# Optimization experiments

Hardware: AMD Instinct MI355X
Metric: run time of the kernel (lower is better)

The kernel has to match this reference:

```python
import jax, jax.numpy as jnp
import numpy as np

N = 1_000_000
IN_DIM = 256
HIDDEN = 32
NUM_SEG = 100_000


def setup_inputs() -> dict:
    key = jax.random.key(0)
    ks = jax.random.split(key, 6)
    review_x = jax.random.normal(ks[0], (N, IN_DIM), dtype=jnp.float32)
    Wq = jax.random.normal(ks[1], (IN_DIM, HIDDEN), dtype=jnp.float32) * (1.0 / np.sqrt(IN_DIM))
    bq = jax.random.normal(ks[2], (HIDDEN,), dtype=jnp.float32) * 0.01
    Wk = jax.random.normal(ks[3], (IN_DIM, HIDDEN), dtype=jnp.float32) * (1.0 / np.sqrt(IN_DIM))
    bk = jax.random.normal(ks[4], (HIDDEN,), dtype=jnp.float32) * 0.01
    review_to_rest_idx = jax.random.randint(ks[5], (N,), 0, NUM_SEG, dtype=jnp.int64 if jax.config.jax_enable_x64 else jnp.int32)
    return {
        "review_x": review_x,
        "Wq": Wq,
        "bq": bq,
        "Wk": Wk,
        "bk": bk,
        "review_to_rest_idx": review_to_rest_idx,
        "num_segments": NUM_SEG,
    }


def reference(review_x, Wq, bq, Wk, bk, review_to_rest_idx, num_segments):
    # q/k projections: [N, hidden]
    qv = review_x @ Wq + bq
    kv = review_x @ Wk + bk
    # attention logits per review: [N]
    att = jnp.sum(qv * kv, axis=-1)
    idx = review_to_rest_idx
    # segment softmax (numerically stable): max, exp, sum per restaurant group
    seg_max = jax.ops.segment_max(att, idx, num_segments=num_segments)
    # empty segments yield -inf max; never gathered, but keep finite for safety
    seg_max = jnp.where(jnp.isfinite(seg_max), seg_max, 0.0)
    e = jnp.exp(att - seg_max[idx])
    seg_sum = jax.ops.segment_sum(e, idx, num_segments=num_segments)
    weights = e / seg_sum[idx]
    return weights
```

## Files before the change

### kernel.cpp

```cpp
#include <hip/hip_runtime.h>
#include <hip/hip_fp16.h>
#include <math.h>

#define IN_DIM 256
#define HID 32
#define NSEG 100000
#define ROWB 1024
#define WBUF 16384

typedef _Float16 half8 __attribute__((ext_vector_type(8)));
typedef __fp16  fp16x2 __attribute__((ext_vector_type(2)));
typedef float floatx4 __attribute__((ext_vector_type(4)));

__device__ __forceinline__ void gload_lds16(const float* g, char* l) {
    __builtin_amdgcn_global_load_lds(
        (const __attribute__((address_space(1))) void*)g,
        (__attribute__((address_space(3))) void*)l,
        16, 0, 0);
}

__global__ __launch_bounds__(256, 2) void att_kernel(
    const float* __restrict__ x,
    const float* __restrict__ Wq, const float* __restrict__ bq,
    const float* __restrict__ Wk, const float* __restrict__ bk,
    const int* __restrict__ idx,
    float* __restrict__ e_out, float* __restrict__ segsum,
    int n, int nsub)
{
    extern __shared__ char smem[];

    const int tid = threadIdx.x;
    const int w  = tid >> 6, l = tid & 63;
    const int lr = l & 15,  lg = l >> 4;

    {
        _Float16* BF = (_Float16*)smem;
        const int ks = tid >> 5, lg2 = (tid >> 3) & 3, j = tid & 7;
        const float4* wqr = (const float4*)(Wq + (size_t)tid * HID);
        const float4* wkr = (const float4*)(Wk + (size_t)tid * HID);
#pragma unroll
        for (int i = 0; i < 8; ++i) {
            float4 vq = wqr[i];
            float4 vk = wkr[i];
            float fq[4] = { vq.x, vq.y, vq.z, vq.w };
            float fk[4] = { vk.x, vk.y, vk.z, vk.w };
#pragma unroll
            for (int u2 = 0; u2 < 4; ++u2) {
                int c = i * 4 + u2, cg = c >> 4, cr = c & 15;
                BF[(((cg    ) * 8 + ks) * 64 + lg2 * 16 + cr) * 8 + j] = (_Float16)fq[u2];
                BF[(((cg + 2) * 8 + ks) * 64 + lg2 * 16 + cr) * 8 + j] = (_Float16)fk[u2];
            }
        }
    }
    __syncthreads();
    half8 b[4][8];
    {
        const _Float16* bfl = (const _Float16*)smem + (size_t)l * 8;
#pragma unroll
        for (int cg = 0; cg < 4; ++cg)
#pragma unroll
            for (int ks = 0; ks < 8; ++ks)
                b[cg][ks] = *(const half8*)(bfl + (cg * 8 + ks) * 512);
    }
    __syncthreads();

    const float bq0 = bq[lr], bq1 = bq[lr + 16];
    const float bk0 = bk[lr], bk1 = bk[lr + 16];

    char* const Xw = smem + w * WBUF;
    const char* const Xr = Xw + lr * ROWB;
    const int sw = lr & 7;

    auto stage = [&](int s) {
#pragma unroll
        for (int r = 0; r < 16; ++r) {
            int grow = s * 16 + r;
            if (grow >= n) grow = n - 1;
            const float* src = x + (size_t)grow * IN_DIM + ((l ^ (r & 7)) << 2);
            gload_lds16(src, Xw + r * ROWB);
        }
    };

    const int gw      = blockIdx.x * 4 + w;
    const int gstride = gridDim.x * 4;

    int s = gw;
    if (s >= nsub) return;

    stage(s);

    while (true) {
        asm volatile("s_waitcnt vmcnt(0)" ::: "memory");
        __builtin_amdgcn_sched_barrier(0);

        floatx4 acc0 = {0.f,0.f,0.f,0.f}, acc1 = {0.f,0.f,0.f,0.f};
        floatx4 acc2 = {0.f,0.f,0.f,0.f}, acc3 = {0.f,0.f,0.f,0.f};
#pragma unroll
        for (int ks = 0; ks < 8; ++ks) {
            float4 v0 = *(const float4*)(Xr + ks * 128 + (((lg * 2 + 0) ^ sw) << 4));
            float4 v1 = *(const float4*)(Xr + ks * 128 + (((lg * 2 + 1) ^ sw) << 4));
            union { half8 h8; fp16x2 h2[4]; } u;
            u.h2[0] = __builtin_amdgcn_cvt_pkrtz(v0.x, v0.y);
            u.h2[1] = __builtin_amdgcn_cvt_pkrtz(v0.z, v0.w);
            u.h2[2] = __builtin_amdgcn_cvt_pkrtz(v1.x, v1.y);
            u.h2[3] = __builtin_amdgcn_cvt_pkrtz(v1.z, v1.w);
            acc0 = __builtin_amdgcn_mfma_f32_16x16x32_f16(u.h8, b[0][ks], acc0, 0, 0, 0);
            acc1 = __builtin_amdgcn_mfma_f32_16x16x32_f16(u.h8, b[1][ks], acc1, 0, 0, 0);
            acc2 = __builtin_amdgcn_mfma_f32_16x16x32_f16(u.h8, b[2][ks], acc2, 0, 0, 0);
            acc3 = __builtin_amdgcn_mfma_f32_16x16x32_f16(u.h8, b[3][ks], acc3, 0, 0, 0);
        }

        float p[4];
#pragma unroll
        for (int i2 = 0; i2 < 4; ++i2) {
            p[i2] = (acc0[i2] + bq0) * (acc2[i2] + bk0)
                  + (acc1[i2] + bq1) * (acc3[i2] + bk1);
            p[i2] += __shfl_xor(p[i2], 1);
            p[i2] += __shfl_xor(p[i2], 2);
            p[i2] += __shfl_xor(p[i2], 4);
            p[i2] += __shfl_xor(p[i2], 8);
        }

        const int snext = s + gstride;

        asm volatile("s_waitcnt lgkmcnt(0)" ::: "memory");
        __builtin_amdgcn_sched_barrier(0);

        if (snext < nsub) stage(snext);

        if (lr < 4) {
            float pv = (lr & 1) ? ((lr & 2) ? p[3] : p[1])
                                : ((lr & 2) ? p[2] : p[0]);
            int r = s * 16 + lg * 4 + lr;
            if (r < n) {
                float e = __expf(pv);
                e_out[r] = e;
                atomicAdd(&segsum[idx[r]], e);
            }
        }

        if (snext >= nsub) break;
        s = snext;
    }
}

__global__ __launch_bounds__(256) void norm_kernel(
    const int* __restrict__ idx, const float* __restrict__ segsum,
    float* __restrict__ out, int n)
{
    int i = blockIdx.x * blockDim.x + threadIdx.x;
    int stride = gridDim.x * blockDim.x;
    int n4 = n >> 2;
    for (; i < n4; i += stride) {
        float4 e = ((const float4*)out)[i];
        int4  s4 = ((const int4*)idx)[i];
        float4 r;
        r.x = e.x / segsum[s4.x];
        r.y = e.y / segsum[s4.y];
        r.z = e.z / segsum[s4.z];
        r.w = e.w / segsum[s4.w];
        ((float4*)out)[i] = r;
    }
    if (blockIdx.x == 0 && threadIdx.x < (n & 3)) {
        int j = (n & ~3) + threadIdx.x;
        out[j] = out[j] / segsum[idx[j]];
    }
}

extern "C" void kernel_launch(void* const* d_in, const int* in_sizes, int n_in,
                              void* d_out, int out_size, void* d_ws, size_t ws_size,
                              hipStream_t stream)
{
    const float* x   = (const float*)d_in[0];
    const float* Wq  = (const float*)d_in[1];
    const float* bq  = (const float*)d_in[2];
    const float* Wk  = (const float*)d_in[3];
    const float* bk  = (const float*)d_in[4];
    const int*   idx = (const int*)d_in[5];
    const int n = in_sizes[5];

    float* segsum = (float*)d_ws;

    (void)hipMemsetAsync(segsum, 0, (size_t)NSEG * 4, stream);

    const int nsub = (n + 15) >> 4;
    int grid1 = 512;
    if (grid1 * 4 > nsub) grid1 = (nsub + 3) / 4;
    att_kernel<<<grid1, 256, 65536, stream>>>(x, Wq, bq, Wk, bk, idx,
                                              (float*)d_out, segsum, n, nsub);

    int n4 = n >> 2;
    int grid2 = (n4 + 255) / 256;
    if (grid2 > 1024) grid2 = 1024;
    if (grid2 < 1) grid2 = 1;
    norm_kernel<<<grid2, 256, 0, stream>>>(idx, segsum, (float*)d_out, n);
}
```

Before: 222.6 us.

## Load activations directly into registers with a software prefetch instead of LDS staging

Replaces the global-to-LDS async staging of x rows with direct global loads into a 16-entry float4 register buffer. The next subtile is prefetched into registers after the current one is converted to fp16. This drops 64KB of dynamic shared memory and the LDS read/wait round trip. In exchange it raises register pressure, and each lane now reads two strided 32-byte chunks per row, which may lower coalescing efficiency.

```diff
diff --git a/kernel.cpp b/kernel.cpp
--- a/kernel.cpp
+++ b/kernel.cpp
@@ -5,19 +5,10 @@
 #define IN_DIM 256
 #define HID 32
 #define NSEG 100000
-#define ROWB 1024
-#define WBUF 16384
 
 typedef _Float16 half8 __attribute__((ext_vector_type(8)));
 typedef __fp16  fp16x2 __attribute__((ext_vector_type(2)));
 typedef float floatx4 __attribute__((ext_vector_type(4)));
-
-__device__ __forceinline__ void gload_lds16(const float* g, char* l) {
-    __builtin_amdgcn_global_load_lds(
-        (const __attribute__((address_space(1))) void*)g,
-        (__attribute__((address_space(3))) void*)l,
-        16, 0, 0);
-}
 
 __global__ __launch_bounds__(256, 2) void att_kernel(
     const float* __restrict__ x,
@@ -27,14 +18,13 @@
     float* __restrict__ e_out, float* __restrict__ segsum,
     int n, int nsub)
 {
-    extern __shared__ char smem[];
+    __shared__ _Float16 BF[4 * 8 * 64 * 8];
 
     const int tid = threadIdx.x;
     const int w  = tid >> 6, l = tid & 63;
     const int lr = l & 15,  lg = l >> 4;
 
     {
-        _Float16* BF = (_Float16*)smem;
         const int ks = tid >> 5, lg2 = (tid >> 3) & 3, j = tid & 7;
         const float4* wqr = (const float4*)(Wq + (size_t)tid * HID);
         const float4* wkr = (const float4*)(Wk + (size_t)tid * HID);
@@ -55,31 +45,16 @@
     __syncthreads();
     half8 b[4][8];
     {
-        const _Float16* bfl = (const _Float16*)smem + (size_t)l * 8;
+        const _Float16* bfl = BF + (size_t)l * 8;
 #pragma unroll
         for (int cg = 0; cg < 4; ++cg)
 #pragma unroll
             for (int ks = 0; ks < 8; ++ks)
                 b[cg][ks] = *(const half8*)(bfl + (cg * 8 + ks) * 512);
     }
-    __syncthreads();
 
     const float bq0 = bq[lr], bq1 = bq[lr + 16];
     const float bk0 = bk[lr], bk1 = bk[lr + 16];
-
-    char* const Xw = smem + w * WBUF;
-    const char* const Xr = Xw + lr * ROWB;
-    const int sw = lr & 7;
-
-    auto stage = [&](int s) {
-#pragma unroll
-        for (int r = 0; r < 16; ++r) {
-            int grow = s * 16 + r;
-            if (grow >= n) grow = n - 1;
-            const float* src = x + (size_t)grow * IN_DIM + ((l ^ (r & 7)) << 2);
-            gload_lds16(src, Xw + r * ROWB);
-        }
-    };
 
     const int gw      = blockIdx.x * 4 + w;
     const int gstride = gridDim.x * 4;
@@ -87,27 +62,51 @@
     int s = gw;
     if (s >= nsub) return;
 
-    stage(s);
+    float4 raw[16];
+    {
+        int row = s * 16 + lr; if (row >= n) row = n - 1;
+        const float* xp = x + (size_t)row * IN_DIM + lg * 8;
+#pragma unroll
+        for (int ks = 0; ks < 8; ++ks) {
+            raw[2 * ks]     = *(const float4*)(xp + ks * 32);
+            raw[2 * ks + 1] = *(const float4*)(xp + ks * 32 + 4);
+        }
+    }
 
     while (true) {
-        asm volatile("s_waitcnt vmcnt(0)" ::: "memory");
+        const int snext = s + gstride;
+
+        half8 a[8];
+#pragma unroll
+        for (int ks = 0; ks < 8; ++ks) {
+            float4 v0 = raw[2 * ks], v1 = raw[2 * ks + 1];
+            union { half8 h8; fp16x2 h2[4]; } u;
+            u.h2[0] = __builtin_amdgcn_cvt_pkrtz(v0.x, v0.y);
+            u.h2[1] = __builtin_amdgcn_cvt_pkrtz(v0.z, v0.w);
+            u.h2[2] = __builtin_amdgcn_cvt_pkrtz(v1.x, v1.y);
+            u.h2[3] = __builtin_amdgcn_cvt_pkrtz(v1.z, v1.w);
+            a[ks] = u.h8;
+        }
+
+        if (snext < nsub) {
+            int row = snext * 16 + lr; if (row >= n) row = n - 1;
+            const float* xp = x + (size_t)row * IN_DIM + lg * 8;
+#pragma unroll
+            for (int ks = 0; ks < 8; ++ks) {
+                raw[2 * ks]     = *(const float4*)(xp + ks * 32);
+                raw[2 * ks + 1] = *(const float4*)(xp + ks * 32 + 4);
+            }
+        }
         __builtin_amdgcn_sched_barrier(0);
 
         floatx4 acc0 = {0.f,0.f,0.f,0.f}, acc1 = {0.f,0.f,0.f,0.f};
         floatx4 acc2 = {0.f,0.f,0.f,0.f}, acc3 = {0.f,0.f,0.f,0.f};
 #pragma unroll
         for (int ks = 0; ks < 8; ++ks) {
-            float4 v0 = *(const float4*)(Xr + ks * 128 + (((lg * 2 + 0) ^ sw) << 4));
-            float4 v1 = *(const float4*)(Xr + ks * 128 + (((lg * 2 + 1) ^ sw) << 4));
-            union { half8 h8; fp16x2 h2[4]; } u;
-            u.h2[0] = __builtin_amdgcn_cvt_pkrtz(v0.x, v0.y);
-            u.h2[1] = __builtin_amdgcn_cvt_pkrtz(v0.z, v0.w);
-            u.h2[2] = __builtin_amdgcn_cvt_pkrtz(v1.x, v1.y);
-            u.h2[3] = __builtin_amdgcn_cvt_pkrtz(v1.z, v1.w);
-            acc0 = __builtin_amdgcn_mfma_f32_16x16x32_f16(u.h8, b[0][ks], acc0, 0, 0, 0);
-            acc1 = __builtin_amdgcn_mfma_f32_16x16x32_f16(u.h8, b[1][ks], acc1, 0, 0, 0);
-            acc2 = __builtin_amdgcn_mfma_f32_16x16x32_f16(u.h8, b[2][ks], acc2, 0, 0, 0);
-            acc3 = __builtin_amdgcn_mfma_f32_16x16x32_f16(u.h8, b[3][ks], acc3, 0, 0, 0);
+            acc0 = __builtin_amdgcn_mfma_f32_16x16x32_f16(a[ks], b[0][ks], acc0, 0, 0, 0);
+            acc1 = __builtin_amdgcn_mfma_f32_16x16x32_f16(a[ks], b[1][ks], acc1, 0, 0, 0);
+            acc2 = __builtin_amdgcn_mfma_f32_16x16x32_f16(a[ks], b[2][ks], acc2, 0, 0, 0);
+            acc3 = __builtin_amdgcn_mfma_f32_16x16x32_f16(a[ks], b[3][ks], acc3, 0, 0, 0);
         }
 
         float p[4];
@@ -120,13 +119,6 @@
             p[i2] += __shfl_xor(p[i2], 4);
             p[i2] += __shfl_xor(p[i2], 8);
         }
-
-        const int snext = s + gstride;
-
-        asm volatile("s_waitcnt lgkmcnt(0)" ::: "memory");
-        __builtin_amdgcn_sched_barrier(0);
-
-        if (snext < nsub) stage(snext);
 
         if (lr < 4) {
             float pv = (lr & 1) ? ((lr & 2) ? p[3] : p[1])
@@ -186,8 +178,8 @@
     const int nsub = (n + 15) >> 4;
     int grid1 = 512;
     if (grid1 * 4 > nsub) grid1 = (nsub + 3) / 4;
-    att_kernel<<<grid1, 256, 65536, stream>>>(x, Wq, bq, Wk, bk, idx,
-                                              (float*)d_out, segsum, n, nsub);
+    att_kernel<<<grid1, 256, 0, stream>>>(x, Wq, bq, Wk, bk, idx,
+                                          (float*)d_out, segsum, n, nsub);
 
     int n4 = n >> 2;
     int grid2 = (n4 + 255) / 256;
```

Result: slower. 244.8 us (+10.0%).

## Double-buffer per-wave LDS staging with 2-wave blocks and early idx prefetch

Applied to the files above, without the earlier changes.

Each block now has two waves instead of four, and each wave gets two 16 KB LDS buffers. The next 16-row tile is issued into the alternate buffer before the MFMA compute on the current tile starts, so global-to-LDS loads overlap compute instead of following it. The segment index for the epilogue is loaded before compute, which keeps that load off the atomic path. The trade-off is half as many resident waves per CU and fewer total waves in the grid, on a kernel that is already close to HBM-bandwidth-bound.

```diff
diff --git a/kernel.cpp b/kernel.cpp
--- a/kernel.cpp
+++ b/kernel.cpp
@@ -19,7 +19,7 @@
         16, 0, 0);
 }
 
-__global__ __launch_bounds__(256, 2) void att_kernel(
+__global__ __launch_bounds__(128) void att_kernel(
     const float* __restrict__ x,
     const float* __restrict__ Wq, const float* __restrict__ bq,
     const float* __restrict__ Wk, const float* __restrict__ bk,
@@ -35,20 +35,24 @@
 
     {
         _Float16* BF = (_Float16*)smem;
-        const int ks = tid >> 5, lg2 = (tid >> 3) & 3, j = tid & 7;
-        const float4* wqr = (const float4*)(Wq + (size_t)tid * HID);
-        const float4* wkr = (const float4*)(Wk + (size_t)tid * HID);
-#pragma unroll
-        for (int i = 0; i < 8; ++i) {
-            float4 vq = wqr[i];
-            float4 vk = wkr[i];
-            float fq[4] = { vq.x, vq.y, vq.z, vq.w };
-            float fk[4] = { vk.x, vk.y, vk.z, vk.w };
-#pragma unroll
-            for (int u2 = 0; u2 < 4; ++u2) {
-                int c = i * 4 + u2, cg = c >> 4, cr = c & 15;
-                BF[(((cg    ) * 8 + ks) * 64 + lg2 * 16 + cr) * 8 + j] = (_Float16)fq[u2];
-                BF[(((cg + 2) * 8 + ks) * 64 + lg2 * 16 + cr) * 8 + j] = (_Float16)fk[u2];
+#pragma unroll
+        for (int rr = 0; rr < 2; ++rr) {
+            const int k = tid + rr * 128;
+            const int ks = k >> 5, lg2 = (k >> 3) & 3, j = k & 7;
+            const float4* wqr = (const float4*)(Wq + (size_t)k * HID);
+            const float4* wkr = (const float4*)(Wk + (size_t)k * HID);
+#pragma unroll
+            for (int i = 0; i < 8; ++i) {
+                float4 vq = wqr[i];
+                float4 vk = wkr[i];
+                float fq[4] = { vq.x, vq.y, vq.z, vq.w };
+                float fk[4] = { vk.x, vk.y, vk.z, vk.w };
+#pragma unroll
+                for (int u2 = 0; u2 < 4; ++u2) {
+                    int c = i * 4 + u2, cg = c >> 4, cr = c & 15;
+                    BF[(((cg    ) * 8 + ks) * 64 + lg2 * 16 + cr) * 8 + j] = (_Float16)fq[u2];
+                    BF[(((cg + 2) * 8 + ks) * 64 + lg2 * 16 + cr) * 8 + j] = (_Float16)fk[u2];
+                }
             }
         }
     }
@@ -67,32 +71,44 @@
     const float bq0 = bq[lr], bq1 = bq[lr + 16];
     const float bk0 = bk[lr], bk1 = bk[lr + 16];
 
-    char* const Xw = smem + w * WBUF;
-    const char* const Xr = Xw + lr * ROWB;
+    char* const Xw = smem + w * (2 * WBUF);
     const int sw = lr & 7;
 
-    auto stage = [&](int s) {
+    auto stage = [&](int s, int bufsel) {
+        char* buf = Xw + bufsel * WBUF;
 #pragma unroll
         for (int r = 0; r < 16; ++r) {
             int grow = s * 16 + r;
             if (grow >= n) grow = n - 1;
             const float* src = x + (size_t)grow * IN_DIM + ((l ^ (r & 7)) << 2);
-            gload_lds16(src, Xw + r * ROWB);
+            gload_lds16(src, buf + r * ROWB);
         }
     };
 
-    const int gw      = blockIdx.x * 4 + w;
-    const int gstride = gridDim.x * 4;
+    const int gw      = blockIdx.x * 2 + w;
+    const int gstride = gridDim.x * 2;
 
     int s = gw;
     if (s >= nsub) return;
 
-    stage(s);
+    int cur = 0;
+    stage(s, cur);
 
     while (true) {
+        const int snext = s + gstride;
+
         asm volatile("s_waitcnt vmcnt(0)" ::: "memory");
         __builtin_amdgcn_sched_barrier(0);
 
+        const int r_ep = s * 16 + lg * 4 + lr;
+        int my_seg = 0;
+        if (lr < 4 && r_ep < n) my_seg = idx[r_ep];
+        __builtin_amdgcn_sched_barrier(0);
+
+        if (snext < nsub) stage(snext, cur ^ 1);
+        __builtin_amdgcn_sched_barrier(0);
+
+        const char* Xr = Xw + cur * WBUF + lr * ROWB;
         floatx4 acc0 = {0.f,0.f,0.f,0.f}, acc1 = {0.f,0.f,0.f,0.f};
         floatx4 acc2 = {0.f,0.f,0.f,0.f}, acc3 = {0.f,0.f,0.f,0.f};
 #pragma unroll
@@ -121,26 +137,20 @@
             p[i2] += __shfl_xor(p[i2], 8);
         }
 
-        const int snext = s + gstride;
-
-        asm volatile("s_waitcnt lgkmcnt(0)" ::: "memory");
-        __builtin_amdgcn_sched_barrier(0);
-
-        if (snext < nsub) stage(snext);
-
-        if (lr < 4) {
+        if (lr < 4 && r_ep < n) {
             float pv = (lr & 1) ? ((lr & 2) ? p[3] : p[1])
                                 : ((lr & 2) ? p[2] : p[0]);
-            int r = s * 16 + lg * 4 + lr;
-            if (r < n) {
-                float e = __expf(pv);
-                e_out[r] = e;
-                atomicAdd(&segsum[idx[r]], e);
-            }
-        }
+            float e = __expf(pv);
+            e_out[r_ep] = e;
+            atomicAdd(&segsum[my_seg], e);
+        }
+
+        asm volatile("s_waitcnt lgkmcnt(0)" ::: "memory");
+        __builtin_amdgcn_sched_barrier(0);
 
         if (snext >= nsub) break;
         s = snext;
+        cur ^= 1;
     }
 }
 
@@ -185,8 +195,8 @@
 
     const int nsub = (n + 15) >> 4;
     int grid1 = 512;
-    if (grid1 * 4 > nsub) grid1 = (nsub + 3) / 4;
-    att_kernel<<<grid1, 256, 65536, stream>>>(x, Wq, bq, Wk, bk, idx,
+    if (grid1 * 2 > nsub) grid1 = (nsub + 1) / 2;
+    att_kernel<<<grid1, 128, 65536, stream>>>(x, Wq, bq, Wk, bk, idx,
                                               (float*)d_out, segsum, n, nsub);
 
     int n4 = n >> 2;
```

Measured after the change: 239.1 us. 7.4% more time.
